# Kernel tuning notes

Measured on AMD Instinct MI355X. Metric: run time of the kernel, lower is better.

The kernel has to match this reference:

```python
import jax, jax.numpy as jnp
import numpy as np

N = 100000
E = 1200000
F_IN = 64
H = 64
PE = 100000
NE = 100000


def setup_inputs() -> dict:
    key = jax.random.key(0)
    ks = jax.random.split(key, 8)
    x = jax.random.normal(ks[0], (N, F_IN), dtype=jnp.float32)
    edge_index = jax.random.randint(ks[1], (2, E), 0, N, dtype=jnp.int64)
    pos_edge_index = jax.random.randint(ks[2], (2, PE), 0, N, dtype=jnp.int64)
    neg_edge_index = jax.random.randint(ks[3], (2, NE), 0, N, dtype=jnp.int64)
    # glorot-ish init for GCNConv linear weights, zero bias (PyG default)
    W1 = jax.random.normal(ks[4], (F_IN, H), dtype=jnp.float32) * (1.0 / np.sqrt(F_IN))
    b1 = jnp.zeros((H,), dtype=jnp.float32)
    W2 = jax.random.normal(ks[5], (H, H), dtype=jnp.float32) * (1.0 / np.sqrt(H))
    b2 = jnp.zeros((H,), dtype=jnp.float32)
    return {"x": x, "edge_index": edge_index, "pos_edge_index": pos_edge_index,
            "neg_edge_index": neg_edge_index, "W1": W1, "b1": b1, "W2": W2, "b2": b2}


def _gcn_norm(edge_index, num_nodes):
    # PyG gcn_norm with add_self_loops=True: deg over col, norm = d^-1/2[row]*d^-1/2[col]
    loop = jnp.arange(num_nodes, dtype=edge_index.dtype)
    src = jnp.concatenate([edge_index[0], loop])
    dst = jnp.concatenate([edge_index[1], loop])
    deg = jax.ops.segment_sum(jnp.ones_like(dst, dtype=jnp.float32), dst,
                              num_segments=num_nodes)
    dis = jnp.where(deg > 0, jax.lax.rsqrt(jnp.maximum(deg, 1.0)), 0.0)
    norm = dis[src] * dis[dst]  # [E+N]
    return src, dst, norm


def _gcn_conv(x, W, b, src, dst, norm, num_nodes):
    h = x @ W                               # [N, H] dense transform first (out_dim small)
    msg = h[src] * norm[:, None]            # gather + scale, [E+N, H]
    out = jax.ops.segment_sum(msg, dst, num_segments=num_nodes)  # scatter-add
    return out + b


def reference(x, edge_index, pos_edge_index, neg_edge_index, W1, b1, W2, b2):
    src, dst, norm = _gcn_norm(edge_index, N)
    z = _gcn_conv(x, W1, b1, src, dst, norm, N)
    z = jax.nn.relu(z)
    z = _gcn_conv(z, W2, b2, src, dst, norm, N)  # [N, H] node embeddings
    # decode: dot product over concatenated pos/neg edge pairs
    ei = jnp.concatenate([pos_edge_index, neg_edge_index], axis=-1)  # [2, PE+NE]
    logits = jnp.sum(z[ei[0]] * z[ei[1]], axis=1)  # [PE+NE]
    return logits
```

## Files before the change

kernel.cpp:

```cpp
#include <hip/hip_runtime.h>

#define NN 100000
#define NE 1200000
#define NPOS 100000
#define NNEG 100000

#define NBUCK ((NN + 255) / 256)
#define BCAP 3712
#define TILE 4096
#define EPT 8

typedef unsigned short bf16_t;

__device__ __forceinline__ float bf2f(bf16_t b) {
    return __uint_as_float(((unsigned int)b) << 16);
}
__device__ __forceinline__ bf16_t f2bf(float f) {
    unsigned int u = __float_as_uint(f);
    u += 0x7FFFu + ((u >> 16) & 1u);
    return (bf16_t)(u >> 16);
}
__device__ __forceinline__ float ulo(unsigned int u) { return bf2f((bf16_t)(u & 0xFFFFu)); }
__device__ __forceinline__ float uhi(unsigned int u) { return bf2f((bf16_t)(u >> 16)); }

__device__ __forceinline__ void acc8(float* a, uint4 u) {
    a[0] += ulo(u.x); a[1] += uhi(u.x);
    a[2] += ulo(u.y); a[3] += uhi(u.y);
    a[4] += ulo(u.z); a[5] += uhi(u.z);
    a[6] += ulo(u.w); a[7] += uhi(u.w);
}

#define GETC(v, i) ((i) == 0 ? (v).x : (i) == 1 ? (v).y : (i) == 2 ? (v).z : (v).w)


__global__ __launch_bounds__(256) void zero_gcur_kernel(int* __restrict__ gcur) {
    int i = blockIdx.x * 256 + threadIdx.x;
    if (i < NBUCK) gcur[i] = 0;
}


__global__ __launch_bounds__(512) void bin_kernel(const int* __restrict__ src,
                                                  const int* __restrict__ dst,
                                                  int* __restrict__ gcur,
                                                  unsigned int* __restrict__ brec) {
    __shared__ int hcnt[NBUCK];
    __shared__ int hbase[NBUCK];
    for (int b = threadIdx.x; b < NBUCK; b += 512) hcnt[b] = 0;
    __syncthreads();

    const int tile0 = blockIdx.x * TILE;
    int bk[EPT];
    int rank[EPT];
    unsigned int rec[EPT];
#pragma unroll
    for (int i = 0; i < EPT; ++i) {
        int e = tile0 + i * 512 + threadIdx.x;
        if (e < NE) {
            int s = src[e];
            int d = dst[e];
            bk[i] = d >> 8;
            rec[i] = ((unsigned int)(d & 255) << 24) | (unsigned int)s;
            rank[i] = atomicAdd(&hcnt[bk[i]], 1);
        } else {
            bk[i] = -1;
        }
    }
    __syncthreads();
    for (int b = threadIdx.x; b < NBUCK; b += 512) {
        int h = hcnt[b];
        if (h > 0) hbase[b] = atomicAdd(&gcur[b], h);
    }
    __syncthreads();
#pragma unroll
    for (int i = 0; i < EPT; ++i) {
        if (bk[i] >= 0) {
            int p = hbase[bk[i]] + rank[i];
            if (p < BCAP) brec[(size_t)bk[i] * BCAP + p] = rec[i];
        }
    }
}


__global__ __launch_bounds__(256) void bucket_csr_kernel(const int* __restrict__ gcur,
                                                         const unsigned int* __restrict__ brec,
                                                         int* __restrict__ csr,
                                                         int* __restrict__ st,
                                                         int* __restrict__ en,
                                                         float* __restrict__ dis) {
    __shared__ int hist[256];
    __shared__ int scanv[256];
    __shared__ int cur[256];
    __shared__ int sorted[BCAP];
    const int b = blockIdx.x;
    const int t = threadIdx.x;
    const int n = min(gcur[b], BCAP);
    const unsigned int* rec = brec + (size_t)b * BCAP;

    hist[t] = 0;
    __syncthreads();
    for (int i = t; i < n; i += 256) atomicAdd(&hist[rec[i] >> 24], 1);
    __syncthreads();

    int c = hist[t];
    scanv[t] = c;
    __syncthreads();
    for (int off = 1; off < 256; off <<= 1) {
        int add = (t >= off) ? scanv[t - off] : 0;
        __syncthreads();
        scanv[t] += add;
        __syncthreads();
    }
    int base = scanv[t] - c;
    cur[t] = base;
    __syncthreads();

    for (int i = t; i < n; i += 256) {
        unsigned int r = rec[i];
        int p = atomicAdd(&cur[r >> 24], 1);
        sorted[p] = (int)(r & 0xFFFFFF);
    }
    __syncthreads();

    for (int i = t; i < n; i += 256) csr[(size_t)b * BCAP + i] = sorted[i];

    int v = b * 256 + t;
    if (v < NN) {
        st[v] = b * BCAP + base;
        en[v] = b * BCAP + base + c;
        dis[v] = rsqrtf((float)(c + 1));
    }
}


__device__ __forceinline__ void gemm_tile_compute(const float4* __restrict__ xs4,
                                                  const float4* __restrict__ ws4,
                                                  int ty, int tx, float acc[4][4]) {
#pragma unroll 2
    for (int k4 = 0; k4 < 16; ++k4) {
        float4 xa0 = xs4[(ty * 4 + 0) * 17 + k4];
        float4 xa1 = xs4[(ty * 4 + 1) * 17 + k4];
        float4 xa2 = xs4[(ty * 4 + 2) * 17 + k4];
        float4 xa3 = xs4[(ty * 4 + 3) * 17 + k4];
        float4 wk0 = ws4[(k4 * 4 + 0) * 16 + tx];
        float4 wk1 = ws4[(k4 * 4 + 1) * 16 + tx];
        float4 wk2 = ws4[(k4 * 4 + 2) * 16 + tx];
        float4 wk3 = ws4[(k4 * 4 + 3) * 16 + tx];
#pragma unroll
        for (int kk = 0; kk < 4; ++kk) {
            float4 wv = (kk == 0) ? wk0 : (kk == 1) ? wk1 : (kk == 2) ? wk2 : wk3;
            float x0 = GETC(xa0, kk), x1 = GETC(xa1, kk);
            float x2 = GETC(xa2, kk), x3 = GETC(xa3, kk);
            acc[0][0] += x0 * wv.x; acc[0][1] += x0 * wv.y; acc[0][2] += x0 * wv.z; acc[0][3] += x0 * wv.w;
            acc[1][0] += x1 * wv.x; acc[1][1] += x1 * wv.y; acc[1][2] += x1 * wv.z; acc[1][3] += x1 * wv.w;
            acc[2][0] += x2 * wv.x; acc[2][1] += x2 * wv.y; acc[2][2] += x2 * wv.z; acc[2][3] += x2 * wv.w;
            acc[3][0] += x3 * wv.x; acc[3][1] += x3 * wv.y; acc[3][2] += x3 * wv.z; acc[3][3] += x3 * wv.w;
        }
    }
}


__global__ __launch_bounds__(256) void gemm64_f32in_kernel(const float* __restrict__ X,
                                                           const float* __restrict__ W,
                                                           const float* __restrict__ dis,
                                                           bf16_t* __restrict__ Hout, int n) {
    __shared__ float4 xs4[64 * 17];
    __shared__ float4 ws4[64 * 16];
    const int tx = threadIdx.x & 15;
    const int ty = threadIdx.x >> 4;
    const int row0 = blockIdx.x * 64;

    const float4* X4 = reinterpret_cast<const float4*>(X + (size_t)row0 * 64);
    const float4* W4 = reinterpret_cast<const float4*>(W);

#pragma unroll
    for (int i = 0; i < 4; ++i) {
        int idx = threadIdx.x + i * 256;
        int r = idx >> 4, c4 = idx & 15;
        int row = row0 + r;
        xs4[r * 17 + c4] = (row < n) ? X4[idx] : make_float4(0.f, 0.f, 0.f, 0.f);
        ws4[idx] = W4[idx];
    }
    __syncthreads();

    float acc[4][4] = {};
    gemm_tile_compute(xs4, ws4, ty, tx, acc);

#pragma unroll
    for (int r = 0; r < 4; ++r) {
        int rw = row0 + ty * 4 + r;
        if (rw < n) {
            float d = dis[rw];
            unsigned int lo = (unsigned int)f2bf(acc[r][0] * d) |
                              ((unsigned int)f2bf(acc[r][1] * d) << 16);
            unsigned int hi = (unsigned int)f2bf(acc[r][2] * d) |
                              ((unsigned int)f2bf(acc[r][3] * d) << 16);
            uint2 u; u.x = lo; u.y = hi;
            *reinterpret_cast<uint2*>(&Hout[(size_t)rw * 64 + tx * 4]) = u;
        }
    }
}


__global__ __launch_bounds__(256) void gemm64_bf16in_kernel(const bf16_t* __restrict__ X,
                                                            const float* __restrict__ W,
                                                            const float* __restrict__ dis,
                                                            bf16_t* __restrict__ Hout, int n) {
    __shared__ float4 xs4[64 * 17];
    __shared__ float4 ws4[64 * 16];
    const int tx = threadIdx.x & 15;
    const int ty = threadIdx.x >> 4;
    const int row0 = blockIdx.x * 64;

    const uint4* X4 = reinterpret_cast<const uint4*>(X + (size_t)row0 * 64);
    const float4* W4 = reinterpret_cast<const float4*>(W);

#pragma unroll
    for (int i = 0; i < 2; ++i) {
        int idx = threadIdx.x + i * 256;
        int r = idx >> 3, c8 = idx & 7;
        int row = row0 + r;
        uint4 u = (row < n) ? X4[idx] : make_uint4(0u, 0u, 0u, 0u);
        float4 v0, v1;
        v0.x = fmaxf(ulo(u.x), 0.f); v0.y = fmaxf(uhi(u.x), 0.f);
        v0.z = fmaxf(ulo(u.y), 0.f); v0.w = fmaxf(uhi(u.y), 0.f);
        v1.x = fmaxf(ulo(u.z), 0.f); v1.y = fmaxf(uhi(u.z), 0.f);
        v1.z = fmaxf(ulo(u.w), 0.f); v1.w = fmaxf(uhi(u.w), 0.f);
        xs4[r * 17 + c8 * 2]     = v0;
        xs4[r * 17 + c8 * 2 + 1] = v1;
    }
#pragma unroll
    for (int i = 0; i < 4; ++i) {
        int idx = threadIdx.x + i * 256;
        ws4[idx] = W4[idx];
    }
    __syncthreads();

    float acc[4][4] = {};
    gemm_tile_compute(xs4, ws4, ty, tx, acc);

#pragma unroll
    for (int r = 0; r < 4; ++r) {
        int rw = row0 + ty * 4 + r;
        if (rw < n) {
            float d = dis[rw];
            unsigned int lo = (unsigned int)f2bf(acc[r][0] * d) |
                              ((unsigned int)f2bf(acc[r][1] * d) << 16);
            unsigned int hi = (unsigned int)f2bf(acc[r][2] * d) |
                              ((unsigned int)f2bf(acc[r][3] * d) << 16);
            uint2 u; u.x = lo; u.y = hi;
            *reinterpret_cast<uint2*>(&Hout[(size_t)rw * 64 + tx * 4]) = u;
        }
    }
}


__global__ __launch_bounds__(256) void agg_kernel(const int* __restrict__ csr,
                                                  const int* __restrict__ st,
                                                  const int* __restrict__ en,
                                                  const float* __restrict__ dis,
                                                  const uint4* __restrict__ Hp8,
                                                  const float* __restrict__ bias,
                                                  uint4* __restrict__ Z8, int n) {
    const int lane = threadIdx.x & 63;
    const int g = lane >> 3;
    const int fl = lane & 7;
    int v = blockIdx.x * 32 + ((threadIdx.x >> 6) << 3) + g;
    const bool act = v < n;
    if (!act) v = n - 1;

    int e = st[v];
    const int e1 = en[v];

    float a0[8] = {}, a1[8] = {}, a2[8] = {}, a3[8] = {};
    acc8(a0, Hp8[(size_t)v * 8 + fl]);

    for (; e + 4 <= e1; e += 4) {
        int s0 = csr[e];
        int s1 = csr[e + 1];
        int s2 = csr[e + 2];
        int s3 = csr[e + 3];
        uint4 u0 = Hp8[(size_t)s0 * 8 + fl];
        uint4 u1 = Hp8[(size_t)s1 * 8 + fl];
        uint4 u2 = Hp8[(size_t)s2 * 8 + fl];
        uint4 u3 = Hp8[(size_t)s3 * 8 + fl];
        acc8(a0, u0);
        acc8(a1, u1);
        acc8(a2, u2);
        acc8(a3, u3);
    }
    for (; e < e1; ++e) {
        acc8(a1, Hp8[(size_t)csr[e] * 8 + fl]);
    }

    if (act) {
        float d = dis[v];
        float4 bA = reinterpret_cast<const float4*>(bias)[fl * 2];
        float4 bB = reinterpret_cast<const float4*>(bias)[fl * 2 + 1];
        float z0 = ((a0[0] + a1[0]) + (a2[0] + a3[0])) * d + bA.x;
        float z1 = ((a0[1] + a1[1]) + (a2[1] + a3[1])) * d + bA.y;
        float z2 = ((a0[2] + a1[2]) + (a2[2] + a3[2])) * d + bA.z;
        float z3 = ((a0[3] + a1[3]) + (a2[3] + a3[3])) * d + bA.w;
        float z4 = ((a0[4] + a1[4]) + (a2[4] + a3[4])) * d + bB.x;
        float z5 = ((a0[5] + a1[5]) + (a2[5] + a3[5])) * d + bB.y;
        float z6 = ((a0[6] + a1[6]) + (a2[6] + a3[6])) * d + bB.z;
        float z7 = ((a0[7] + a1[7]) + (a2[7] + a3[7])) * d + bB.w;
        uint4 u;
        u.x = (unsigned int)f2bf(z0) | ((unsigned int)f2bf(z1) << 16);
        u.y = (unsigned int)f2bf(z2) | ((unsigned int)f2bf(z3) << 16);
        u.z = (unsigned int)f2bf(z4) | ((unsigned int)f2bf(z5) << 16);
        u.w = (unsigned int)f2bf(z6) | ((unsigned int)f2bf(z7) << 16);
        Z8[(size_t)v * 8 + fl] = u;
    }
}


__global__ __launch_bounds__(256) void decode_kernel(const int* __restrict__ pos,
                                                     const int* __restrict__ neg,
                                                     const uint4* __restrict__ Z8,
                                                     float* __restrict__ out) {
    const int lane = threadIdx.x & 63;
    const int fl = lane & 7;
    const int pair = blockIdx.x * 32 + ((threadIdx.x >> 6) << 3) + (lane >> 3);
    if (pair >= NPOS + NNEG) return;
    int a, b;
    if (pair < NPOS) {
        a = pos[pair];
        b = pos[NPOS + pair];
    } else {
        int p = pair - NPOS;
        a = neg[p];
        b = neg[NNEG + p];
    }
    uint4 ua = Z8[(size_t)a * 8 + fl];
    uint4 ub = Z8[(size_t)b * 8 + fl];
    float v = ulo(ua.x) * ulo(ub.x) + uhi(ua.x) * uhi(ub.x)
            + ulo(ua.y) * ulo(ub.y) + uhi(ua.y) * uhi(ub.y)
            + ulo(ua.z) * ulo(ub.z) + uhi(ua.z) * uhi(ub.z)
            + ulo(ua.w) * ulo(ub.w) + uhi(ua.w) * uhi(ub.w);
#pragma unroll
    for (int off = 4; off > 0; off >>= 1) v += __shfl_xor(v, off, 64);
    if (fl == 0) out[pair] = v;
}


__global__ __launch_bounds__(256) void init_deg_kernel(float* __restrict__ deg, int n) {
    int i = blockIdx.x * 256 + threadIdx.x;
    if (i < n) deg[i] = 1.0f;
}
__global__ __launch_bounds__(256) void deg_count_kernel(const int* __restrict__ dst,
                                                        float* __restrict__ deg, int e) {
    int i = blockIdx.x * 256 + threadIdx.x;
    if (i < e) atomicAdd(&deg[dst[i]], 1.0f);
}
__global__ __launch_bounds__(256) void dis_kernel(float* __restrict__ deg, int n) {
    int i = blockIdx.x * 256 + threadIdx.x;
    if (i < n) deg[i] = rsqrtf(deg[i]);
}
template <bool RELU>
__global__ __launch_bounds__(256) void gemm64_f32out_kernel(const float* __restrict__ X,
                                                            const float* __restrict__ W,
                                                            float* __restrict__ Hout, int n) {
    __shared__ float xs[64][64];
    const int lane = threadIdx.x & 63;
    const int wid = threadIdx.x >> 6;
    float w[64];
#pragma unroll
    for (int k = 0; k < 64; ++k) w[k] = W[k * 64 + lane];
    const int row0 = blockIdx.x * 64;
#pragma unroll
    for (int i = 0; i < 16; ++i) {
        int idx = threadIdx.x + i * 256;
        int r = idx >> 6, c = idx & 63;
        int row = row0 + r;
        float v = (row < n) ? X[(size_t)row * 64 + c] : 0.0f;
        if (RELU) v = fmaxf(v, 0.0f);
        xs[r][c] = v;
    }
    __syncthreads();
#pragma unroll 1
    for (int rr = 0; rr < 16; ++rr) {
        int r = wid * 16 + rr;
        int row = row0 + r;
        if (row < n) {
            float acc = 0.0f;
#pragma unroll
            for (int k = 0; k < 64; ++k) acc += xs[r][k] * w[k];
            Hout[(size_t)row * 64 + lane] = acc;
        }
    }
}
__global__ __launch_bounds__(256) void selfloop_init_kernel(const float* __restrict__ H,
                                                            const float* __restrict__ dis,
                                                            const float* __restrict__ b,
                                                            float* __restrict__ Z, int n) {
    int i = blockIdx.x * 256 + threadIdx.x;
    if (i < n * 16) {
        int v = i >> 4, c = i & 15;
        float d = dis[v], d2 = d * d;
        float4 h4 = reinterpret_cast<const float4*>(H)[i];
        float4 b4 = reinterpret_cast<const float4*>(b)[c];
        float4 z4;
        z4.x = b4.x + h4.x * d2;
        z4.y = b4.y + h4.y * d2;
        z4.z = b4.z + h4.z * d2;
        z4.w = b4.w + h4.w * d2;
        reinterpret_cast<float4*>(Z)[i] = z4;
    }
}
__global__ __launch_bounds__(256) void edge_agg_kernel(const int* __restrict__ src,
                                                       const int* __restrict__ dst,
                                                       const float* __restrict__ dis,
                                                       const float* __restrict__ H,
                                                       float* __restrict__ Z, int e) {
    const int lane = threadIdx.x & 63;
    const int edge = blockIdx.x * 4 + (threadIdx.x >> 6);
    if (edge < e) {
        int s = src[edge];
        int d = dst[edge];
        float nm = dis[s] * dis[d];
        float v = H[(size_t)s * 64 + lane] * nm;
        atomicAdd(&Z[(size_t)d * 64 + lane], v);
    }
}
__global__ __launch_bounds__(256) void decode_f32_kernel(const int* __restrict__ pos,
                                                         const int* __restrict__ neg,
                                                         const float* __restrict__ Z,
                                                         float* __restrict__ out) {
    const int lane = threadIdx.x & 63;
    const int pair = blockIdx.x * 4 + (threadIdx.x >> 6);
    if (pair >= NPOS + NNEG) return;
    int a, b;
    if (pair < NPOS) {
        a = pos[pair];
        b = pos[NPOS + pair];
    } else {
        int p = pair - NPOS;
        a = neg[p];
        b = neg[NNEG + p];
    }
    float v = Z[(size_t)a * 64 + lane] * Z[(size_t)b * 64 + lane];
#pragma unroll
    for (int off = 32; off > 0; off >>= 1) v += __shfl_down(v, off, 64);
    if (lane == 0) out[pair] = v;
}


extern "C" void kernel_launch(void* const* d_in, const int* in_sizes, int n_in,
                              void* d_out, int out_size, void* d_ws, size_t ws_size,
                              hipStream_t stream) {
    const float* x   = (const float*)d_in[0];
    const int*   ei  = (const int*)d_in[1];
    const int*   pos = (const int*)d_in[2];
    const int*   neg = (const int*)d_in[3];
    const float* W1  = (const float*)d_in[4];
    const float* b1  = (const float*)d_in[5];
    const float* W2  = (const float*)d_in[6];
    const float* b2  = (const float*)d_in[7];
    float* out = (float*)d_out;

    const int* src = ei;
    const int* dst = ei + NE;

    char* ws = (char*)d_ws;
    size_t o = 0;
    auto alloc = [&](size_t bytes) {
        size_t p = o;
        o = (o + bytes + 255) & ~(size_t)255;
        return p;
    };
    float*        dis  = (float*)(ws + alloc((size_t)NN * 4));
    int*          gcur = (int*)(ws + alloc((size_t)NBUCK * 4));
    unsigned int* brec = (unsigned int*)(ws + alloc((size_t)NBUCK * BCAP * 4));
    int*          csr  = (int*)(ws + alloc((size_t)NBUCK * BCAP * 4));
    int*          stA  = (int*)(ws + alloc((size_t)NN * 4));
    int*          enA  = (int*)(ws + alloc((size_t)NN * 4));
    bf16_t*       bufA = (bf16_t*)(ws + alloc((size_t)NN * 64 * 2));
    bf16_t*       bufB = (bf16_t*)(ws + alloc((size_t)NN * 64 * 2));

    if (o <= ws_size) {
        zero_gcur_kernel<<<(NBUCK + 255) / 256, 256, 0, stream>>>(gcur);
        bin_kernel<<<(NE + TILE - 1) / TILE, 512, 0, stream>>>(src, dst, gcur, brec);
        bucket_csr_kernel<<<NBUCK, 256, 0, stream>>>(gcur, brec, csr, stA, enA, dis);

        gemm64_f32in_kernel<<<(NN + 63) / 64, 256, 0, stream>>>(x, W1, dis, bufA, NN);
        agg_kernel<<<(NN + 31) / 32, 256, 0, stream>>>(csr, stA, enA, dis,
                                                       (const uint4*)bufA, b1,
                                                       (uint4*)bufB, NN);

        gemm64_bf16in_kernel<<<(NN + 63) / 64, 256, 0, stream>>>(bufB, W2, dis, bufA, NN);
        agg_kernel<<<(NN + 31) / 32, 256, 0, stream>>>(csr, stA, enA, dis,
                                                       (const uint4*)bufA, b2,
                                                       (uint4*)bufB, NN);

        decode_kernel<<<((NPOS + NNEG) + 31) / 32, 256, 0, stream>>>(pos, neg,
                                                                     (const uint4*)bufB, out);
    } else {
        float* fdis = (float*)ws;
        size_t foff = ((size_t)NN * 4 + 255) / 256 * 256;
        float* fA = (float*)(ws + foff);
        float* fB = fA + (size_t)NN * 64;

        init_deg_kernel<<<(NN + 255) / 256, 256, 0, stream>>>(fdis, NN);
        deg_count_kernel<<<(NE + 255) / 256, 256, 0, stream>>>(dst, fdis, NE);
        dis_kernel<<<(NN + 255) / 256, 256, 0, stream>>>(fdis, NN);

        gemm64_f32out_kernel<false><<<(NN + 63) / 64, 256, 0, stream>>>(x, W1, fA, NN);
        selfloop_init_kernel<<<(NN * 16 + 255) / 256, 256, 0, stream>>>(fA, fdis, b1, fB, NN);
        edge_agg_kernel<<<(NE + 3) / 4, 256, 0, stream>>>(src, dst, fdis, fA, fB, NE);

        gemm64_f32out_kernel<true><<<(NN + 63) / 64, 256, 0, stream>>>(fB, W2, fA, NN);
        selfloop_init_kernel<<<(NN * 16 + 255) / 256, 256, 0, stream>>>(fA, fdis, b2, fB, NN);
        edge_agg_kernel<<<(NE + 3) / 4, 256, 0, stream>>>(src, dst, fdis, fA, fB, NE);

        decode_f32_kernel<<<((NPOS + NNEG) + 3) / 4, 256, 0, stream>>>(pos, neg, fB, out);
    }
}
```

Before: 137.3 us.

## Fuse layer-1 aggregation with layer-2 GEMM and halve binning tile size

Replaces the separate layer-1 aggregation kernel and the bf16-input GEMM with one kernel. It gathers neighbour rows, applies bias and ReLU, stages the 32-row result in shared memory, then multiplies by W2 and scales by the degree normaliser. This removes one kernel launch and the write and re-read of the intermediate activation buffer. The binning tile and edges-per-thread are also halved, giving more binning blocks. In exchange, each fused block only feeds 32 rows into the GEMM and has to load W2 itself.

Result: faster. 129.6 us, median of 2 (-5.6%).

```diff
diff --git a/kernel.cpp b/kernel.cpp
--- a/kernel.cpp
+++ b/kernel.cpp
@@ -7,8 +7,8 @@
 
 #define NBUCK ((NN + 255) / 256)
 #define BCAP 3712
-#define TILE 4096
-#define EPT 8
+#define TILE 2048
+#define EPT 4
 
 typedef unsigned short bf16_t;
 
@@ -158,7 +158,6 @@
     }
 }
 
-
 __global__ __launch_bounds__(256) void gemm64_f32in_kernel(const float* __restrict__ X,
                                                            const float* __restrict__ W,
                                                            const float* __restrict__ dis,
@@ -201,46 +200,89 @@
 }
 
 
-__global__ __launch_bounds__(256) void gemm64_bf16in_kernel(const bf16_t* __restrict__ X,
-                                                            const float* __restrict__ W,
-                                                            const float* __restrict__ dis,
-                                                            bf16_t* __restrict__ Hout, int n) {
-    __shared__ float4 xs4[64 * 17];
+__global__ __launch_bounds__(256) void agg_gemm_kernel(const int* __restrict__ csr,
+                                                       const int* __restrict__ st,
+                                                       const int* __restrict__ en,
+                                                       const float* __restrict__ dis,
+                                                       const uint4* __restrict__ Hp8,
+                                                       const float* __restrict__ bias,
+                                                       const float* __restrict__ W2,
+                                                       bf16_t* __restrict__ Hout, int n) {
+    __shared__ float4 zs4[32 * 17];
     __shared__ float4 ws4[64 * 16];
+    const int lane = threadIdx.x & 63;
+    const int g = lane >> 3;
+    const int fl = lane & 7;
+    const int v0 = blockIdx.x * 32;
+    const int lrow = ((threadIdx.x >> 6) << 3) + g;
+    int v = v0 + lrow;
+    if (v >= n) v = n - 1;
+
+    const float4* W4 = reinterpret_cast<const float4*>(W2);
+#pragma unroll
+    for (int i = 0; i < 4; ++i) ws4[threadIdx.x + i * 256] = W4[threadIdx.x + i * 256];
+
+    int e = st[v];
+    const int e1 = en[v];
+    float a0[8] = {}, a1[8] = {}, a2[8] = {}, a3[8] = {};
+    acc8(a0, Hp8[(size_t)v * 8 + fl]);
+
+    for (; e + 4 <= e1; e += 4) {
+        int s0 = csr[e];
+        int s1 = csr[e + 1];
+        int s2 = csr[e + 2];
+        int s3 = csr[e + 3];
+        uint4 u0 = Hp8[(size_t)s0 * 8 + fl];
+        uint4 u1 = Hp8[(size_t)s1 * 8 + fl];
+        uint4 u2 = Hp8[(size_t)s2 * 8 + fl];
+        uint4 u3 = Hp8[(size_t)s3 * 8 + fl];
+        acc8(a0, u0);
+        acc8(a1, u1);
+        acc8(a2, u2);
+        acc8(a3, u3);
+    }
+    for (; e < e1; ++e) acc8(a1, Hp8[(size_t)csr[e] * 8 + fl]);
+
+    {
+        float d = dis[v];
+        float4 bA = reinterpret_cast<const float4*>(bias)[fl * 2];
+        float4 bB = reinterpret_cast<const float4*>(bias)[fl * 2 + 1];
+        float4 zA, zB;
+        zA.x = fmaxf(((a0[0] + a1[0]) + (a2[0] + a3[0])) * d + bA.x, 0.f);
+        zA.y = fmaxf(((a0[1] + a1[1]) + (a2[1] + a3[1])) * d + bA.y, 0.f);
+        zA.z = fmaxf(((a0[2] + a1[2]) + (a2[2] + a3[2])) * d + bA.z, 0.f);
+        zA.w = fmaxf(((a0[3] + a1[3]) + (a2[3] + a3[3])) * d + bA.w, 0.f);
+        zB.x = fmaxf(((a0[4] + a1[4]) + (a2[4] + a3[4])) * d + bB.x, 0.f);
+        zB.y = fmaxf(((a0[5] + a1[5]) + (a2[5] + a3[5])) * d + bB.y, 0.f);
+        zB.z = fmaxf(((a0[6] + a1[6]) + (a2[6] + a3[6])) * d + bB.z, 0.f);
+        zB.w = fmaxf(((a0[7] + a1[7]) + (a2[7] + a3[7])) * d + bB.w, 0.f);
+        zs4[lrow * 17 + fl * 2]     = zA;
+        zs4[lrow * 17 + fl * 2 + 1] = zB;
+    }
+    __syncthreads();
+
     const int tx = threadIdx.x & 15;
     const int ty = threadIdx.x >> 4;
-    const int row0 = blockIdx.x * 64;
-
-    const uint4* X4 = reinterpret_cast<const uint4*>(X + (size_t)row0 * 64);
-    const float4* W4 = reinterpret_cast<const float4*>(W);
-
-#pragma unroll
-    for (int i = 0; i < 2; ++i) {
-        int idx = threadIdx.x + i * 256;
-        int r = idx >> 3, c8 = idx & 7;
-        int row = row0 + r;
-        uint4 u = (row < n) ? X4[idx] : make_uint4(0u, 0u, 0u, 0u);
-        float4 v0, v1;
-        v0.x = fmaxf(ulo(u.x), 0.f); v0.y = fmaxf(uhi(u.x), 0.f);
-        v0.z = fmaxf(ulo(u.y), 0.f); v0.w = fmaxf(uhi(u.y), 0.f);
-        v1.x = fmaxf(ulo(u.z), 0.f); v1.y = fmaxf(uhi(u.z), 0.f);
-        v1.z = fmaxf(ulo(u.w), 0.f); v1.w = fmaxf(uhi(u.w), 0.f);
-        xs4[r * 17 + c8 * 2]     = v0;
-        xs4[r * 17 + c8 * 2 + 1] = v1;
-    }
-#pragma unroll
-    for (int i = 0; i < 4; ++i) {
-        int idx = threadIdx.x + i * 256;
-        ws4[idx] = W4[idx];
-    }
-    __syncthreads();
-
-    float acc[4][4] = {};
-    gemm_tile_compute(xs4, ws4, ty, tx, acc);
-
-#pragma unroll
-    for (int r = 0; r < 4; ++r) {
-        int rw = row0 + ty * 4 + r;
+    float acc[2][4] = {};
+#pragma unroll 2
+    for (int k4 = 0; k4 < 16; ++k4) {
+        float4 xa0 = zs4[(ty * 2 + 0) * 17 + k4];
+        float4 xa1 = zs4[(ty * 2 + 1) * 17 + k4];
+        float4 wk0 = ws4[(k4 * 4 + 0) * 16 + tx];
+        float4 wk1 = ws4[(k4 * 4 + 1) * 16 + tx];
+        float4 wk2 = ws4[(k4 * 4 + 2) * 16 + tx];
+        float4 wk3 = ws4[(k4 * 4 + 3) * 16 + tx];
+#pragma unroll
+        for (int kk = 0; kk < 4; ++kk) {
+            float4 wv = (kk == 0) ? wk0 : (kk == 1) ? wk1 : (kk == 2) ? wk2 : wk3;
+            float x0 = GETC(xa0, kk), x1 = GETC(xa1, kk);
+            acc[0][0] += x0 * wv.x; acc[0][1] += x0 * wv.y; acc[0][2] += x0 * wv.z; acc[0][3] += x0 * wv.w;
+            acc[1][0] += x1 * wv.x; acc[1][1] += x1 * wv.y; acc[1][2] += x1 * wv.z; acc[1][3] += x1 * wv.w;
+        }
+    }
+#pragma unroll
+    for (int r = 0; r < 2; ++r) {
+        int rw = v0 + ty * 2 + r;
         if (rw < n) {
             float d = dis[rw];
             unsigned int lo = (unsigned int)f2bf(acc[r][0] * d) |
@@ -483,17 +525,17 @@
         bucket_csr_kernel<<<NBUCK, 256, 0, stream>>>(gcur, brec, csr, stA, enA, dis);
 
         gemm64_f32in_kernel<<<(NN + 63) / 64, 256, 0, stream>>>(x, W1, dis, bufA, NN);
+
+        agg_gemm_kernel<<<(NN + 31) / 32, 256, 0, stream>>>(csr, stA, enA, dis,
+                                                            (const uint4*)bufA, b1, W2,
+                                                            bufB, NN);
+
         agg_kernel<<<(NN + 31) / 32, 256, 0, stream>>>(csr, stA, enA, dis,
-                                                       (const uint4*)bufA, b1,
-                                                       (uint4*)bufB, NN);
-
-        gemm64_bf16in_kernel<<<(NN + 63) / 64, 256, 0, stream>>>(bufB, W2, dis, bufA, NN);
-        agg_kernel<<<(NN + 31) / 32, 256, 0, stream>>>(csr, stA, enA, dis,
-                                                       (const uint4*)bufA, b2,
-                                                       (uint4*)bufB, NN);
+                                                       (const uint4*)bufB, b2,
+                                                       (uint4*)bufA, NN);
 
         decode_kernel<<<((NPOS + NNEG) + 31) / 32, 256, 0, stream>>>(pos, neg,
-                                                                     (const uint4*)bufB, out);
+                                                                     (const uint4*)bufA, out);
     } else {
         float* fdis = (float*)ws;
         size_t foff = ((size_t)NN * 4 + 255) / 256 * 256;
```
